# Optimization experiments

Measured on AMD Instinct MI355X. Metric: run time of the kernel, lower is better.

## Reference

```python
import jax, jax.numpy as jnp
import numpy as np

N = 500_000   # points
K = 16        # top-level components
S = 2         # subcomponents per component
D = 32        # repr_dim
EPS = 1e-10


def setup_inputs() -> dict:
    key = jax.random.key(0)
    k1, k2, k3 = jax.random.split(key, 3)
    X = jax.random.normal(k1, (N, D), dtype=jnp.float32)
    # responsibilities are row-stochastic in the original EM loop
    r = jax.nn.softmax(jax.random.normal(k2, (N, K), dtype=jnp.float32), axis=-1)
    ri = jax.nn.softmax(jax.random.normal(k3, (N, K * S), dtype=jnp.float32), axis=-1)
    return {"X": X, "r": r, "ri": ri}


def _m_step(X, z, ri):
    """Fused segment-reduce M-step: equivalent to the per-cluster python loop
    X_k = X[z==i]; r_k = ri[z==i, S*i:S*(i+1)]; weighted mean/cov per subcomp,
    but computed in one pass via one-hot gating of the responsibilities."""
    n = X.shape[0]
    mask = jax.nn.one_hot(z, K, dtype=X.dtype)                 # [N, K]
    pi = ri.sum(axis=0) / n                                    # [K*S]
    # gate subcluster responsibilities by hard top-level assignment
    w = (ri.reshape(n, K, S) * mask[:, :, None]).reshape(n, K * S)  # [N, K*S]
    denom = w.sum(axis=0)                                      # [K*S]  (= r_k.sum(0) per cluster)
    safe = jnp.maximum(denom, EPS)
    mus = jnp.einsum('nk,nd->kd', w, X) / safe[:, None]        # [K*S, D]
    # weighted second moment per component; loop via lax.map over the small
    # fixed K*S axis to avoid an [N, K*S, D] intermediate
    def second_moment(wk):
        return (X * wk[:, None]).T @ X                         # [D, D]
    m2 = jax.lax.map(second_moment, w.T) / safe[:, None, None] # [K*S, D, D]
    covs = m2 - mus[:, :, None] * mus[:, None, :]              # E[xx^T] - mu mu^T
    return pi, mus, covs


def reference(X, r, ri):
    z = jnp.argmax(r, axis=-1)   # [N] hard top-level assignment
    return _m_step(X, z, ri)
```

## Files before the change

kernel.cpp:

```cpp
#include <hip/hip_runtime.h>

#define AS1 __attribute__((address_space(1)))
#define AS3 __attribute__((address_space(3)))
#define CHUNK 256
#define NB 256
#define PIGRID 2048

typedef unsigned int uint;
typedef unsigned short ushort;
typedef __attribute__((ext_vector_type(4))) float f32x4;
typedef __attribute__((ext_vector_type(8))) _Float16 h8;
typedef __attribute__((ext_vector_type(2))) __fp16 fp16x2;

union H8 { uint u[4]; h8 h; };

__device__ __forceinline__ void gld_lds16(const float* g, float* l) {
  __builtin_amdgcn_global_load_lds((const AS1 void*)g, (AS3 void*)l, 16, 0, 0);
}
__device__ __forceinline__ uint pkrtz(float a, float b) {
  union { fp16x2 h; uint u; } c;
  c.h = __builtin_amdgcn_cvt_pkrtz(a, b);
  return c.u;
}

#define WAITVM0  do { asm volatile("s_waitcnt vmcnt(0)" ::: "memory"); __builtin_amdgcn_sched_barrier(0); } while (0)
#define WAITLGKM do { asm volatile("s_waitcnt lgkmcnt(0)" ::: "memory"); __builtin_amdgcn_sched_barrier(0); } while (0)
#define BAR __builtin_amdgcn_s_barrier()

__global__ __launch_bounds__(256) void fused_k(
    const float* __restrict__ r, const float* __restrict__ ri,
    unsigned char* __restrict__ zb, float* __restrict__ wpairf,
    float* __restrict__ pigp, int n)
{
  __shared__ unsigned char zs[256];
  __shared__ float4 s[256];
  const int t = threadIdx.x;
  const int cg = t & 7;
  const int pr = t >> 3;
  const int ppb = (n + PIGRID - 1) / PIGRID;
  const int p0 = blockIdx.x * ppb;
  const int p1 = min(p0 + ppb, n);
  const float4* rif = (const float4*)ri;

  int px[8]; float msk[8]; float4 rv[8];
#pragma unroll
  for (int j = 0; j < 8; ++j) {
    int p = p0 + pr + j * 32;
    px[j] = p;
    msk[j] = (p < p1) ? 1.f : 0.f;
    int pc = p < p1 ? p : p1 - 1;
    rv[j] = rif[(size_t)pc * 8 + cg];
  }

  int myp = p0 + t;
  if (t < ppb && myp < n) {
    const float4* rr = (const float4*)(r + (size_t)myp * 16);
    float4 a0 = rr[0], a1 = rr[1], a2 = rr[2], a3 = rr[3];
    float best = a0.x; int z = 0;
#define CHK(v, c) if ((v) > best) { best = (v); z = (c); }
    CHK(a0.y,1) CHK(a0.z,2) CHK(a0.w,3)
    CHK(a1.x,4) CHK(a1.y,5) CHK(a1.z,6) CHK(a1.w,7)
    CHK(a2.x,8) CHK(a2.y,9) CHK(a2.z,10) CHK(a2.w,11)
    CHK(a3.x,12) CHK(a3.y,13) CHK(a3.z,14) CHK(a3.w,15)
#undef CHK
    zs[t] = (unsigned char)z;
    zb[myp] = (unsigned char)z;
  }
  __syncthreads();

  float4 acc = make_float4(0.f, 0.f, 0.f, 0.f);
#pragma unroll
  for (int j = 0; j < 8; ++j) {
    float4 v = rv[j];
    float m = msk[j];
    if (m != 0.f) {
      int zv = zs[px[j] - p0];
      if (cg == (zv >> 1)) {
        float2 wp = (zv & 1) ? make_float2(v.z, v.w) : make_float2(v.x, v.y);
        *(float2*)&wpairf[(size_t)px[j] * 2] = wp;
      }
    }
    acc.x += v.x * m; acc.y += v.y * m; acc.z += v.z * m; acc.w += v.w * m;
  }
  s[t] = acc;
  __syncthreads();
  if (t < 8) {
    float4 a = s[t];
#pragma unroll
    for (int q = 1; q < 32; ++q) {
      float4 v = s[t + q * 8];
      a.x += v.x; a.y += v.y; a.z += v.z; a.w += v.w;
    }
    *(float4*)&pigp[blockIdx.x * 32 + t * 4] = a;
  }
}

#define CLUSTER_MFMA(CIDX, T00a,T01a,T11a,T20a,T21a, T00b,T01b,T11b,T20b,T21b) { \
  const int c_ = (CIDX); \
  int cnt_ = lcnt[b][c_]; if (cnt_ > 64) cnt_ = 64; \
  const int ng_ = (cnt_ + 31) >> 5; \
  for (int g_ = 0; g_ < ng_; ++g_) { \
    alignas(16) ushort praw_[8]; \
    *(uint4*)praw_ = *(const uint4*)&list[b][c_][(g_ << 5) + ((l >> 4) << 3)]; \
    const int sbase_ = (g_ << 5) + ((l >> 4) << 3); \
    int p_[8]; \
    _Pragma("unroll") for (int j = 0; j < 8; ++j) \
      p_[j] = (sbase_ + j < cnt_) ? (int)praw_[j] : 256; \
    uint W_[8]; \
    _Pragma("unroll") for (int j = 0; j < 8; ++j) W_[j] = wls[b][p_[j]]; \
    H8 F0_, F1_, ws0_, ws1_; \
    _Pragma("unroll") for (int j = 0; j < 4; ++j) { \
      uint l0 = xh[b][p_[2*j]*34 + c16], l1 = xh[b][p_[2*j+1]*34 + c16]; \
      uint h0 = xh[b][p_[2*j]*34 + 16 + c16], h1 = xh[b][p_[2*j+1]*34 + 16 + c16]; \
      F0_.u[j] = l0 | (l1 << 16); \
      F1_.u[j] = h0 | (h1 << 16); \
      ws0_.u[j] = (W_[2*j] & 0xffffu) | (W_[2*j+1] << 16); \
      ws1_.u[j] = (W_[2*j] >> 16) | (W_[2*j+1] & 0xffff0000u); \
    } \
    H8 s00_, s01_, s10_, s11_, i20_, i21_; \
    s00_.h = F0_.h * ws0_.h; s01_.h = F1_.h * ws0_.h; \
    s10_.h = F0_.h * ws1_.h; s11_.h = F1_.h * ws1_.h; \
    _Pragma("unroll") for (int j = 0; j < 4; ++j) { \
      i20_.u[j] = lane16 ? ws0_.u[j] : 0u; \
      i21_.u[j] = lane16 ? ws1_.u[j] : 0u; \
    } \
    T00a = __builtin_amdgcn_mfma_f32_16x16x32_f16(s00_.h, s00_.h, T00a, 0,0,0); \
    T01a = __builtin_amdgcn_mfma_f32_16x16x32_f16(s00_.h, s01_.h, T01a, 0,0,0); \
    T11a = __builtin_amdgcn_mfma_f32_16x16x32_f16(s01_.h, s01_.h, T11a, 0,0,0); \
    T20a = __builtin_amdgcn_mfma_f32_16x16x32_f16(i20_.h, s00_.h, T20a, 0,0,0); \
    T21a = __builtin_amdgcn_mfma_f32_16x16x32_f16(i20_.h, s01_.h, T21a, 0,0,0); \
    T00b = __builtin_amdgcn_mfma_f32_16x16x32_f16(s10_.h, s10_.h, T00b, 0,0,0); \
    T01b = __builtin_amdgcn_mfma_f32_16x16x32_f16(s10_.h, s11_.h, T01b, 0,0,0); \
    T11b = __builtin_amdgcn_mfma_f32_16x16x32_f16(s11_.h, s11_.h, T11b, 0,0,0); \
    T20b = __builtin_amdgcn_mfma_f32_16x16x32_f16(i21_.h, s10_.h, T20b, 0,0,0); \
    T21b = __builtin_amdgcn_mfma_f32_16x16x32_f16(i21_.h, s11_.h, T21b, 0,0,0); \
  } }

#define STORE_MFMA(COMP, T00,T01,T11,T20,T21) { \
  float* dst_ = m2p + ((size_t)blockIdx.x * 32 + (COMP)) * 768; \
  const int r0_ = (l >> 4) << 2; \
  f32x4 t00_ = T00, t01_ = T01, t11_ = T11; \
  *(float4*)&dst_[c16 * 16 + r0_] = *(float4*)&t00_; \
  *(float4*)&dst_[256 + c16 * 16 + r0_] = *(float4*)&t11_; \
  *(float4*)&dst_[512 + c16 * 16 + r0_] = *(float4*)&t01_; \
  if (l < 16) { \
    musp[((size_t)blockIdx.x * 32 + (COMP)) * 32 + l] = T20[0]; \
    musp[((size_t)blockIdx.x * 32 + (COMP)) * 32 + 16 + l] = T21[0]; \
  } }

__global__ __launch_bounds__(512, 2) void mstep_k(
    const float* __restrict__ X, const unsigned char* __restrict__ zb,
    const float* __restrict__ wpairf,
    float* __restrict__ m2p, float* __restrict__ musp, float* __restrict__ dnp,
    int n, int nchunks)
{
  __shared__ float xf32[CHUNK * 32];
  __shared__ __align__(16) ushort xh[2][257 * 34];
  __shared__ uint wls[2][257];
  __shared__ __align__(16) ushort list[2][16][64];
  __shared__ int lcnt[2][16];
  __shared__ float dn[16][2];

  const int t = threadIdx.x;
  const int wv = t >> 6;
  const int l = t & 63;
  const int c16 = l & 15;
  const bool lane16 = (l & 15) == 0;
  const int G = gridDim.x;

  f32x4 z4 = {0.f, 0.f, 0.f, 0.f};
  f32x4 a0_00=z4, a0_01=z4, a0_11=z4, a0_20=z4, a0_21=z4;
  f32x4 b0_00=z4, b0_01=z4, b0_11=z4, b0_20=z4, b0_21=z4;
  f32x4 a1_00=z4, a1_01=z4, a1_11=z4, a1_20=z4, a1_21=z4;
  f32x4 b1_00=z4, b1_01=z4, b1_11=z4, b1_20=z4, b1_21=z4;

  float wr0 = 0.f, wr1 = 0.f; int zr = 0;

  auto STAGEX = [&](int ch) {
#pragma unroll
    for (int q = 0; q < 4; ++q) {
      int gi = ch * CHUNK + wv * 32 + q * 8 + (l >> 3);
      if (gi > n - 1) gi = n - 1;
      gld_lds16(X + (size_t)gi * 32 + ((l & 7) << 2), &xf32[(wv * 32 + q * 8) * 32]);
    }
  };
  auto LOADWZ = [&](int ch) {
    if (t < CHUNK) {
      int gi = ch * CHUNK + t;
      if (gi < n) {
        float2 w2 = *(const float2*)(wpairf + (size_t)gi * 2);
        wr0 = w2.x; wr1 = w2.y; zr = zb[gi];
      } else { wr0 = 0.f; wr1 = 0.f; zr = 0; }
    }
  };
  auto CVT = [&](int nb) {
    const int p = t >> 1, hh = t & 1;
    const float4* s4 = (const float4*)(xf32 + p * 32 + hh * 16);
    uint* dst = (uint*)&xh[nb][p * 34 + hh * 16];
#pragma unroll
    for (int i = 0; i < 4; ++i) {
      int ii = (i + p) & 3;
      float4 v = s4[ii];
      dst[2 * ii]     = pkrtz(v.x, v.y);
      dst[2 * ii + 1] = pkrtz(v.z, v.w);
    }
    if (t < CHUNK) {
      wls[nb][t] = pkrtz(sqrtf(wr0), sqrtf(wr1));
      atomicAdd(&dn[zr][0], wr0);
      atomicAdd(&dn[zr][1], wr1);
      int pos = atomicAdd(&lcnt[nb][zr], 1);
      if (pos < 64) list[nb][zr][pos] = (ushort)t;
    }
  };

  if (t < 32) ((int*)lcnt)[t] = 0;
  if (t < 32) ((float*)dn)[t] = 0.f;
  if (t < 17) {
    ((uint*)&xh[0][256 * 34])[t] = 0;
    ((uint*)&xh[1][256 * 34])[t] = 0;
  }
  if (t == 0) { wls[0][256] = 0; wls[1][256] = 0; }

  int ch = blockIdx.x;
  int b = 0;
  if (ch < nchunks) {
    STAGEX(ch); LOADWZ(ch);
    WAITVM0; WAITLGKM; BAR;
    CVT(0);
    WAITLGKM; BAR;
    if (ch + G < nchunks) { STAGEX(ch + G); LOADWZ(ch + G); }
    while (true) {
      CLUSTER_MFMA(wv * 2 + 0, a0_00,a0_01,a0_11,a0_20,a0_21,
                               b0_00,b0_01,b0_11,b0_20,b0_21)
      CLUSTER_MFMA(wv * 2 + 1, a1_00,a1_01,a1_11,a1_20,a1_21,
                               b1_00,b1_01,b1_11,b1_20,b1_21)
      int chn = ch + G;
      if (chn >= nchunks) break;
      WAITVM0; WAITLGKM; BAR;
      if (t < 16) lcnt[b][t] = 0;
      CVT(b ^ 1);
      WAITLGKM; BAR;
      if (chn + G < nchunks) { STAGEX(chn + G); LOADWZ(chn + G); }
      b ^= 1; ch = chn;
    }
  }

  STORE_MFMA((wv * 2 + 0) * 2 + 0, a0_00,a0_01,a0_11,a0_20,a0_21)
  STORE_MFMA((wv * 2 + 0) * 2 + 1, b0_00,b0_01,b0_11,b0_20,b0_21)
  STORE_MFMA((wv * 2 + 1) * 2 + 0, a1_00,a1_01,a1_11,a1_20,a1_21)
  STORE_MFMA((wv * 2 + 1) * 2 + 1, b1_00,b1_01,b1_11,b1_20,b1_21)
  if (t < 32) dnp[blockIdx.x * 32 + t] = dn[t >> 1][t & 1];
}

__global__ __launch_bounds__(256) void reduce_k(
    const float* __restrict__ m2p, const float* __restrict__ musp,
    const float* __restrict__ dnp, const float* __restrict__ pigp,
    float* __restrict__ m2r, float* __restrict__ musr,
    float* __restrict__ dnr, float* __restrict__ pigr8, int nb)
{
  const int t = threadIdx.x;
  const int bid = blockIdx.x;

  if (bid < 200) {
    __shared__ float4 red[256];
    const float* in; float* outp; int rs, colbase;
    if (bid < 192) { in = m2p;  outp = m2r;  rs = 24576; colbase = bid * 32; }
    else           { in = musp; outp = musr; rs = 1024;  colbase = (bid - 192) * 32; }
    const int col = colbase + (t & 31);
    float4 a = make_float4(0.f, 0.f, 0.f, 0.f);
#pragma unroll 4
    for (int bb = t >> 5; bb < nb; bb += 8) {
      float4 v = *(const float4*)&in[(size_t)bb * rs + col * 4];
      a.x += v.x; a.y += v.y; a.z += v.z; a.w += v.w;
    }
    red[t] = a;
    __syncthreads();
    if (t < 32) {
      float4 s = red[t];
#pragma unroll
      for (int q = 1; q < 8; ++q) {
        float4 v = red[t + q * 32];
        s.x += v.x; s.y += v.y; s.z += v.z; s.w += v.w;
      }
      *(float4*)&outp[col * 4] = s;
    }
  } else {
    __shared__ float redf[256];
    const float* in; float* outp; int rows, row0;
    if (bid == 200) { in = dnp; outp = dnr; rows = nb; row0 = 0; }
    else {
      in = pigp; outp = pigr8 + (bid - 201) * 32;
      rows = PIGRID / 8; row0 = (bid - 201) * (PIGRID / 8);
    }
    float a = 0.f;
    const int c = t & 31;
#pragma unroll 4
    for (int bb = t >> 5; bb < rows; bb += 8) a += in[(row0 + bb) * 32 + c];
    redf[t] = a;
    __syncthreads();
    if (t < 32) {
      float s = redf[t];
#pragma unroll
      for (int q = 1; q < 8; ++q) s += redf[t + q * 32];
      outp[c] = s;
    }
  }
}

__global__ __launch_bounds__(256) void finalize_k(
    const float* __restrict__ pigr8, const float* __restrict__ dnr,
    const float* __restrict__ musr, const float* __restrict__ m2r,
    float* __restrict__ out, int n)
{
  const int c = blockIdx.x;
  const int t = threadIdx.x;
  __shared__ float mu[32];
  float safe = fmaxf(dnr[c], 1e-10f);
  if (t < 32) {
    float m = musr[c * 32 + t] / safe;
    mu[t] = m;
    out[32 + c * 32 + t] = m;
  }
  if (c == 0 && t < 32) {
    float p = 0.f;
#pragma unroll
    for (int s = 0; s < 8; ++s) p += pigr8[s * 32 + t];
    out[t] = p / (float)n;
  }
  __syncthreads();
  const int d1 = t >> 3;
  const int c0 = (t * 4) & 31;
  const float* base = m2r + c * 768;
  float vals[4];
  if (d1 < 16) {
    if (c0 < 16) {
      float4 v = *(const float4*)&base[d1 * 16 + c0];
      vals[0]=v.x; vals[1]=v.y; vals[2]=v.z; vals[3]=v.w;
    } else {
      int cc = c0 - 16;
#pragma unroll
      for (int j = 0; j < 4; ++j) vals[j] = base[512 + (cc + j) * 16 + d1];
    }
  } else {
    int dd = d1 - 16;
    if (c0 < 16) {
      float4 v = *(const float4*)&base[512 + dd * 16 + c0];
      vals[0]=v.x; vals[1]=v.y; vals[2]=v.z; vals[3]=v.w;
    } else {
      float4 v = *(const float4*)&base[256 + dd * 16 + (c0 - 16)];
      vals[0]=v.x; vals[1]=v.y; vals[2]=v.z; vals[3]=v.w;
    }
  }
  float mud1 = mu[d1];
  float4 cov;
  cov.x = vals[0] / safe - mud1 * mu[c0 + 0];
  cov.y = vals[1] / safe - mud1 * mu[c0 + 1];
  cov.z = vals[2] / safe - mud1 * mu[c0 + 2];
  cov.w = vals[3] / safe - mud1 * mu[c0 + 3];
  *(float4*)&out[32 + 1024 + c * 1024 + t * 4] = cov;
}

extern "C" void kernel_launch(void* const* d_in, const int* in_sizes, int n_in,
                              void* d_out, int out_size, void* d_ws, size_t ws_size,
                              hipStream_t stream) {
  const float* X  = (const float*)d_in[0];
  const float* r  = (const float*)d_in[1];
  const float* ri = (const float*)d_in[2];
  float* out = (float*)d_out;
  const int n = in_sizes[0] / 32;
  const int nchunks = (n + CHUNK - 1) / CHUNK;

  float* m2p   = (float*)d_ws;
  float* musp  = m2p + (size_t)NB * 32 * 768;
  float* dnp   = musp + (size_t)NB * 32 * 32;
  float* m2r   = dnp + (size_t)NB * 32;
  float* musr  = m2r + 24576;
  float* dnr   = musr + 1024;
  float* pigr8 = dnr + 32;
  float* pigp  = pigr8 + 8 * 32;
  float* wpair = pigp + (size_t)PIGRID * 32;
  unsigned char* zbuf = (unsigned char*)(wpair + 2 * (size_t)n);

  fused_k<<<PIGRID, 256, 0, stream>>>(r, ri, zbuf, wpair, pigp, n);
  mstep_k<<<NB, 512, 0, stream>>>(X, zbuf, wpair, m2p, musp, dnp, n, nchunks);
  reduce_k<<<209, 256, 0, stream>>>(m2p, musp, dnp, pigp, m2r, musr, dnr, pigr8, NB);
  finalize_k<<<32, 256, 0, stream>>>(pigr8, dnr, musr, m2r, out, n);
}
```

Measured before the change: 60.44 us.

## Fuse argmax and pi reduction into M-step kernel, dropping the preprocessing pass

Removes the separate fused_k kernel that computed argmax labels, gated weight pairs and pi partial sums. The M-step kernel now streams r and ri per chunk itself, staging ri into LDS with async global-to-LDS loads and accumulating pi sums in registers. This avoids writing and re-reading the intermediate z and weight-pair buffers and saves one launch. In exchange, LDS use grows, occupancy drops to one block per CU, the X fp16 buffer is single-buffered, and the pipeline is restructured so the next chunk's loads overlap the MFMA work.

```diff
diff --git a/kernel.cpp b/kernel.cpp
--- a/kernel.cpp
+++ b/kernel.cpp
@@ -4,7 +4,6 @@
 #define AS3 __attribute__((address_space(3)))
 #define CHUNK 256
 #define NB 256
-#define PIGRID 2048
 
 typedef unsigned int uint;
 typedef unsigned short ushort;
@@ -27,91 +26,23 @@
 #define WAITLGKM do { asm volatile("s_waitcnt lgkmcnt(0)" ::: "memory"); __builtin_amdgcn_sched_barrier(0); } while (0)
 #define BAR __builtin_amdgcn_s_barrier()
 
-__global__ __launch_bounds__(256) void fused_k(
-    const float* __restrict__ r, const float* __restrict__ ri,
-    unsigned char* __restrict__ zb, float* __restrict__ wpairf,
-    float* __restrict__ pigp, int n)
-{
-  __shared__ unsigned char zs[256];
-  __shared__ float4 s[256];
-  const int t = threadIdx.x;
-  const int cg = t & 7;
-  const int pr = t >> 3;
-  const int ppb = (n + PIGRID - 1) / PIGRID;
-  const int p0 = blockIdx.x * ppb;
-  const int p1 = min(p0 + ppb, n);
-  const float4* rif = (const float4*)ri;
-
-  int px[8]; float msk[8]; float4 rv[8];
-#pragma unroll
-  for (int j = 0; j < 8; ++j) {
-    int p = p0 + pr + j * 32;
-    px[j] = p;
-    msk[j] = (p < p1) ? 1.f : 0.f;
-    int pc = p < p1 ? p : p1 - 1;
-    rv[j] = rif[(size_t)pc * 8 + cg];
-  }
-
-  int myp = p0 + t;
-  if (t < ppb && myp < n) {
-    const float4* rr = (const float4*)(r + (size_t)myp * 16);
-    float4 a0 = rr[0], a1 = rr[1], a2 = rr[2], a3 = rr[3];
-    float best = a0.x; int z = 0;
-#define CHK(v, c) if ((v) > best) { best = (v); z = (c); }
-    CHK(a0.y,1) CHK(a0.z,2) CHK(a0.w,3)
-    CHK(a1.x,4) CHK(a1.y,5) CHK(a1.z,6) CHK(a1.w,7)
-    CHK(a2.x,8) CHK(a2.y,9) CHK(a2.z,10) CHK(a2.w,11)
-    CHK(a3.x,12) CHK(a3.y,13) CHK(a3.z,14) CHK(a3.w,15)
-#undef CHK
-    zs[t] = (unsigned char)z;
-    zb[myp] = (unsigned char)z;
-  }
-  __syncthreads();
-
-  float4 acc = make_float4(0.f, 0.f, 0.f, 0.f);
-#pragma unroll
-  for (int j = 0; j < 8; ++j) {
-    float4 v = rv[j];
-    float m = msk[j];
-    if (m != 0.f) {
-      int zv = zs[px[j] - p0];
-      if (cg == (zv >> 1)) {
-        float2 wp = (zv & 1) ? make_float2(v.z, v.w) : make_float2(v.x, v.y);
-        *(float2*)&wpairf[(size_t)px[j] * 2] = wp;
-      }
-    }
-    acc.x += v.x * m; acc.y += v.y * m; acc.z += v.z * m; acc.w += v.w * m;
-  }
-  s[t] = acc;
-  __syncthreads();
-  if (t < 8) {
-    float4 a = s[t];
-#pragma unroll
-    for (int q = 1; q < 32; ++q) {
-      float4 v = s[t + q * 8];
-      a.x += v.x; a.y += v.y; a.z += v.z; a.w += v.w;
-    }
-    *(float4*)&pigp[blockIdx.x * 32 + t * 4] = a;
-  }
-}
-
-#define CLUSTER_MFMA(CIDX, T00a,T01a,T11a,T20a,T21a, T00b,T01b,T11b,T20b,T21b) { \
+#define CLUSTER_MFMA(CIDX, B, T00a,T01a,T11a,T20a,T21a, T00b,T01b,T11b,T20b,T21b) { \
   const int c_ = (CIDX); \
-  int cnt_ = lcnt[b][c_]; if (cnt_ > 64) cnt_ = 64; \
+  int cnt_ = lcnt[B][c_]; if (cnt_ > 64) cnt_ = 64; \
   const int ng_ = (cnt_ + 31) >> 5; \
   for (int g_ = 0; g_ < ng_; ++g_) { \
     alignas(16) ushort praw_[8]; \
-    *(uint4*)praw_ = *(const uint4*)&list[b][c_][(g_ << 5) + ((l >> 4) << 3)]; \
+    *(uint4*)praw_ = *(const uint4*)&list[B][c_][(g_ << 5) + ((l >> 4) << 3)]; \
     const int sbase_ = (g_ << 5) + ((l >> 4) << 3); \
     int p_[8]; \
     _Pragma("unroll") for (int j = 0; j < 8; ++j) \
       p_[j] = (sbase_ + j < cnt_) ? (int)praw_[j] : 256; \
     uint W_[8]; \
-    _Pragma("unroll") for (int j = 0; j < 8; ++j) W_[j] = wls[b][p_[j]]; \
+    _Pragma("unroll") for (int j = 0; j < 8; ++j) W_[j] = wls[B][p_[j]]; \
     H8 F0_, F1_, ws0_, ws1_; \
     _Pragma("unroll") for (int j = 0; j < 4; ++j) { \
-      uint l0 = xh[b][p_[2*j]*34 + c16], l1 = xh[b][p_[2*j+1]*34 + c16]; \
-      uint h0 = xh[b][p_[2*j]*34 + 16 + c16], h1 = xh[b][p_[2*j+1]*34 + 16 + c16]; \
+      uint l0 = xh[p_[2*j]*34 + c16], l1 = xh[p_[2*j+1]*34 + c16]; \
+      uint h0 = xh[p_[2*j]*34 + 16 + c16], h1 = xh[p_[2*j+1]*34 + 16 + c16]; \
       F0_.u[j] = l0 | (l1 << 16); \
       F1_.u[j] = h0 | (h1 << 16); \
       ws0_.u[j] = (W_[2*j] & 0xffffu) | (W_[2*j+1] << 16); \
@@ -148,14 +79,15 @@
     musp[((size_t)blockIdx.x * 32 + (COMP)) * 32 + 16 + l] = T21[0]; \
   } }
 
-__global__ __launch_bounds__(512, 2) void mstep_k(
-    const float* __restrict__ X, const unsigned char* __restrict__ zb,
-    const float* __restrict__ wpairf,
+__global__ __launch_bounds__(512, 1) void giant_k(
+    const float* __restrict__ X, const float* __restrict__ r,
+    const float* __restrict__ ri,
     float* __restrict__ m2p, float* __restrict__ musp, float* __restrict__ dnp,
-    int n, int nchunks)
+    float* __restrict__ pigp, int n, int nchunks)
 {
   __shared__ float xf32[CHUNK * 32];
-  __shared__ __align__(16) ushort xh[2][257 * 34];
+  __shared__ float ril[CHUNK * 32];
+  __shared__ __align__(16) ushort xh[257 * 34];
   __shared__ uint wls[2][257];
   __shared__ __align__(16) ushort list[2][16][64];
   __shared__ int lcnt[2][16];
@@ -173,8 +105,8 @@
   f32x4 b0_00=z4, b0_01=z4, b0_11=z4, b0_20=z4, b0_21=z4;
   f32x4 a1_00=z4, a1_01=z4, a1_11=z4, a1_20=z4, a1_21=z4;
   f32x4 b1_00=z4, b1_01=z4, b1_11=z4, b1_20=z4, b1_21=z4;
-
-  float wr0 = 0.f, wr1 = 0.f; int zr = 0;
+  float4 ppi = make_float4(0.f, 0.f, 0.f, 0.f);
+  float4 rA = ppi, rB = ppi, rC = ppi, rD = ppi;
 
   auto STAGEX = [&](int ch) {
 #pragma unroll
@@ -184,63 +116,84 @@
       gld_lds16(X + (size_t)gi * 32 + ((l & 7) << 2), &xf32[(wv * 32 + q * 8) * 32]);
     }
   };
-  auto LOADWZ = [&](int ch) {
+  auto STAGERI = [&](int ch) {
+#pragma unroll
+    for (int q = 0; q < 4; ++q) {
+      int gi = ch * CHUNK + wv * 32 + q * 8 + (l >> 3);
+      if (gi > n - 1) gi = n - 1;
+      gld_lds16(ri + (size_t)gi * 32 + ((l & 7) << 2), &ril[(wv * 32 + q * 8) * 32]);
+    }
+  };
+  auto LOADR = [&](int ch) {
     if (t < CHUNK) {
       int gi = ch * CHUNK + t;
-      if (gi < n) {
-        float2 w2 = *(const float2*)(wpairf + (size_t)gi * 2);
-        wr0 = w2.x; wr1 = w2.y; zr = zb[gi];
-      } else { wr0 = 0.f; wr1 = 0.f; zr = 0; }
+      if (gi > n - 1) gi = n - 1;
+      const float4* rr = (const float4*)(r + (size_t)gi * 16);
+      rA = rr[0]; rB = rr[1]; rC = rr[2]; rD = rr[3];
     }
   };
-  auto CVT = [&](int nb) {
-    const int p = t >> 1, hh = t & 1;
-    const float4* s4 = (const float4*)(xf32 + p * 32 + hh * 16);
-    uint* dst = (uint*)&xh[nb][p * 34 + hh * 16];
-#pragma unroll
-    for (int i = 0; i < 4; ++i) {
-      int ii = (i + p) & 3;
-      float4 v = s4[ii];
-      dst[2 * ii]     = pkrtz(v.x, v.y);
-      dst[2 * ii + 1] = pkrtz(v.z, v.w);
-    }
-    if (t < CHUNK) {
-      wls[nb][t] = pkrtz(sqrtf(wr0), sqrtf(wr1));
-      atomicAdd(&dn[zr][0], wr0);
-      atomicAdd(&dn[zr][1], wr1);
-      int pos = atomicAdd(&lcnt[nb][zr], 1);
-      if (pos < 64) list[nb][zr][pos] = (ushort)t;
+  auto PREP = [&](int ch, int b) {
+    int rem = n - ch * CHUNK; if (rem > CHUNK) rem = CHUNK;
+    {
+      const int p = t >> 1, hh = t & 1;
+      const float4* s4c = (const float4*)(xf32 + p * 32 + hh * 16);
+      uint* dst = (uint*)&xh[p * 34 + hh * 16];
+#pragma unroll
+      for (int i = 0; i < 4; ++i) {
+        int ii = (i + p) & 3;
+        float4 v = s4c[ii];
+        dst[2 * ii]     = pkrtz(v.x, v.y);
+        dst[2 * ii + 1] = pkrtz(v.z, v.w);
+      }
+    }
+    if (t < rem) {
+      float best = rA.x; int z = 0;
+#define CHK(v, c) if ((v) > best) { best = (v); z = (c); }
+      CHK(rA.y,1) CHK(rA.z,2) CHK(rA.w,3)
+      CHK(rB.x,4) CHK(rB.y,5) CHK(rB.z,6) CHK(rB.w,7)
+      CHK(rC.x,8) CHK(rC.y,9) CHK(rC.z,10) CHK(rC.w,11)
+      CHK(rD.x,12) CHK(rD.y,13) CHK(rD.z,14) CHK(rD.w,15)
+#undef CHK
+      float2 w2 = *(const float2*)&ril[t * 32 + 2 * z];
+      wls[b][t] = pkrtz(sqrtf(w2.x), sqrtf(w2.y));
+      atomicAdd(&dn[z][0], w2.x);
+      atomicAdd(&dn[z][1], w2.y);
+      int pos = atomicAdd(&lcnt[b][z], 1);
+      if (pos < 64) list[b][z][pos] = (ushort)t;
+    }
+    if (t < 16) lcnt[b ^ 1][t] = 0;
+    const float4* r4 = (const float4*)ril;
+#pragma unroll
+    for (int k = 0; k < 4; ++k) {
+      int fi = t + k * 512;
+      if ((fi >> 3) < rem) {
+        float4 v = r4[fi];
+        ppi.x += v.x; ppi.y += v.y; ppi.z += v.z; ppi.w += v.w;
+      }
     }
   };
 
-  if (t < 32) ((int*)lcnt)[t] = 0;
-  if (t < 32) ((float*)dn)[t] = 0.f;
-  if (t < 17) {
-    ((uint*)&xh[0][256 * 34])[t] = 0;
-    ((uint*)&xh[1][256 * 34])[t] = 0;
-  }
+  if (t < 32) { ((int*)lcnt)[t] = 0; ((float*)dn)[t] = 0.f; }
+  if (t < 17) ((uint*)&xh[256 * 34])[t] = 0;
   if (t == 0) { wls[0][256] = 0; wls[1][256] = 0; }
 
   int ch = blockIdx.x;
   int b = 0;
   if (ch < nchunks) {
-    STAGEX(ch); LOADWZ(ch);
+    STAGEX(ch); STAGERI(ch); LOADR(ch);
     WAITVM0; WAITLGKM; BAR;
-    CVT(0);
-    WAITLGKM; BAR;
-    if (ch + G < nchunks) { STAGEX(ch + G); LOADWZ(ch + G); }
     while (true) {
-      CLUSTER_MFMA(wv * 2 + 0, a0_00,a0_01,a0_11,a0_20,a0_21,
-                               b0_00,b0_01,b0_11,b0_20,b0_21)
-      CLUSTER_MFMA(wv * 2 + 1, a1_00,a1_01,a1_11,a1_20,a1_21,
-                               b1_00,b1_01,b1_11,b1_20,b1_21)
+      PREP(ch, b);
+      WAITLGKM; BAR;
       int chn = ch + G;
+      if (chn < nchunks) { STAGEX(chn); STAGERI(chn); LOADR(chn); }
+      CLUSTER_MFMA(wv * 2 + 0, b, a0_00,a0_01,a0_11,a0_20,a0_21,
+                                  b0_00,b0_01,b0_11,b0_20,b0_21)
+      CLUSTER_MFMA(wv * 2 + 1, b, a1_00,a1_01,a1_11,a1_20,a1_21,
+                                  b1_00,b1_01,b1_11,b1_20,b1_21)
       if (chn >= nchunks) break;
-      WAITVM0; WAITLGKM; BAR;
-      if (t < 16) lcnt[b][t] = 0;
-      CVT(b ^ 1);
-      WAITLGKM; BAR;
-      if (chn + G < nchunks) { STAGEX(chn + G); LOADWZ(chn + G); }
+      BAR;
+      WAITVM0;
       b ^= 1; ch = chn;
     }
   }
@@ -250,6 +203,20 @@
   STORE_MFMA((wv * 2 + 1) * 2 + 0, a1_00,a1_01,a1_11,a1_20,a1_21)
   STORE_MFMA((wv * 2 + 1) * 2 + 1, b1_00,b1_01,b1_11,b1_20,b1_21)
   if (t < 32) dnp[blockIdx.x * 32 + t] = dn[t >> 1][t & 1];
+
+  __syncthreads();
+  float4* s4 = (float4*)ril;
+  s4[t] = ppi;
+  __syncthreads();
+  if (t < 8) {
+    float4 a = s4[t];
+#pragma unroll
+    for (int q = 1; q < 64; ++q) {
+      float4 v = s4[t + q * 8];
+      a.x += v.x; a.y += v.y; a.z += v.z; a.w += v.w;
+    }
+    *(float4*)&pigp[blockIdx.x * 32 + t * 4] = a;
+  }
 }
 
 __global__ __launch_bounds__(256) void reduce_k(
@@ -290,7 +257,7 @@
     if (bid == 200) { in = dnp; outp = dnr; rows = nb; row0 = 0; }
     else {
       in = pigp; outp = pigr8 + (bid - 201) * 32;
-      rows = PIGRID / 8; row0 = (bid - 201) * (PIGRID / 8);
+      rows = nb / 8; row0 = (bid - 201) * (nb / 8);
     }
     float a = 0.f;
     const int c = t & 31;
@@ -378,11 +345,8 @@
   float* dnr   = musr + 1024;
   float* pigr8 = dnr + 32;
   float* pigp  = pigr8 + 8 * 32;
-  float* wpair = pigp + (size_t)PIGRID * 32;
-  unsigned char* zbuf = (unsigned char*)(wpair + 2 * (size_t)n);
-
-  fused_k<<<PIGRID, 256, 0, stream>>>(r, ri, zbuf, wpair, pigp, n);
-  mstep_k<<<NB, 512, 0, stream>>>(X, zbuf, wpair, m2p, musp, dnp, n, nchunks);
+
+  giant_k<<<NB, 512, 0, stream>>>(X, r, ri, m2p, musp, dnp, pigp, n, nchunks);
   reduce_k<<<209, 256, 0, stream>>>(m2p, musp, dnp, pigp, m2r, musr, dnr, pigr8, NB);
   finalize_k<<<32, 256, 0, stream>>>(pigr8, dnr, musr, m2r, out, n);
 }
```

Result: faster. 53.71 us (median of 2 runs) (-11.1%).
